# Performance work log

Measured on AMD Instinct MI355X. Metric: run time of the kernel, lower is better.

## Reference

```python
import jax, jax.numpy as jnp
import numpy as np

N_MODEL = 1024
N_HEADS = 16
KV_HEADS = 4
HEAD_DIM = N_MODEL // N_HEADS          # 64
KV_MODEL = HEAD_DIM * KV_HEADS         # 256
GROUPS = N_HEADS // KV_HEADS           # 4
B, S = 4, 2048


def _rmsnorm(x):
    return x * jax.lax.rsqrt(jnp.mean(x * x, axis=-1, keepdims=True) + 1e-6)


def _act_quant(x):
    # 8-bit absmax per-token quantization (BitNet b1.58)
    scale = 127.0 / jnp.clip(jnp.max(jnp.abs(x), axis=-1, keepdims=True), 1e-5)
    return jnp.clip(jnp.round(x * scale), -128.0, 127.0) / scale


def _weight_quant(w):
    # ternary absmean quantization
    scale = 1.0 / jnp.clip(jnp.mean(jnp.abs(w)), 1e-5)
    return jnp.clip(jnp.round(w * scale), -1.0, 1.0) / scale


def bitlinear(x, w, b):
    xn = _rmsnorm(x)
    xq = xn + jax.lax.stop_gradient(_act_quant(xn) - xn)   # STE
    wq = w + jax.lax.stop_gradient(_weight_quant(w) - w)   # STE
    return jnp.einsum('...i,oi->...o', xq, wq) + b


def setup_inputs() -> dict:
    key = jax.random.key(0)
    ks = jax.random.split(key, 11)
    sq = 1.0 / np.sqrt(N_MODEL)
    sk = 1.0 / np.sqrt(KV_MODEL)
    return {
        'query': jax.random.normal(ks[0], (B, S, N_MODEL), jnp.float32),
        'key':   jax.random.normal(ks[1], (B, S, N_MODEL), jnp.float32),
        'value': jax.random.normal(ks[2], (B, S, N_MODEL), jnp.float32),
        'Wq': jax.random.normal(ks[3], (N_MODEL, N_MODEL), jnp.float32) * sq,
        'bq': jnp.zeros((N_MODEL,), jnp.float32),
        'Wk': jax.random.normal(ks[4], (KV_MODEL, N_MODEL), jnp.float32) * sq,
        'bk': jnp.zeros((KV_MODEL,), jnp.float32),
        'Wv': jax.random.normal(ks[5], (KV_MODEL, N_MODEL), jnp.float32) * sq,
        'bv': jnp.zeros((KV_MODEL,), jnp.float32),
        'Wo': jax.random.normal(ks[6], (N_MODEL, KV_MODEL), jnp.float32) * sk,
        'bo': jnp.zeros((N_MODEL,), jnp.float32),
    }


def reference(query, key, value, Wq, bq, Wk, bk, Wv, bv, Wo, bo):
    b = query.shape[0]
    Q = bitlinear(query, Wq, bq)   # [b, n, n_model]
    K = bitlinear(key,   Wk, bk)   # [b, s, kv_model]
    V = bitlinear(value, Wv, bv)   # [b, s, kv_model]

    # [b, h, n, d] layouts
    Q = Q.reshape(b, -1, N_HEADS, HEAD_DIM).transpose(0, 2, 1, 3)
    K = K.reshape(b, -1, KV_HEADS, HEAD_DIM).transpose(0, 2, 1, 3)
    V = V.reshape(b, -1, KV_HEADS, HEAD_DIM).transpose(0, 2, 1, 3)

    # group query heads: [b, g, kv_h, n, d]
    Qg = Q.reshape(b, KV_HEADS, GROUPS, -1, HEAD_DIM).transpose(0, 2, 1, 3, 4)
    # NOTE: faithful to the module, the einsum output has no 'g' axis,
    # so the grouped query heads are SUMMED over g.
    energy = jnp.einsum('bghnd,bhsd->bhns', Qg, K)  # [b, kv_h, n, s]

    scale = jnp.sqrt(jnp.float32(HEAD_DIM))
    attention = jax.nn.softmax(energy / scale, axis=-1)
    x = jnp.einsum('bhns,bhsd->bhnd', attention, V)  # [b, kv_h, n, d]
    x = x.transpose(0, 2, 1, 3).reshape(b, -1, KV_MODEL)
    x = bitlinear(x, Wo, bo)       # [b, n, n_model]
    return (x, attention)
```

## Files before the change

### kernel.cpp

```cpp
#include <hip/hip_runtime.h>
#include <stdint.h>

#define N_MODELC 1024
#define KV_MODELC 256
#define BATCH 4
#define SEQ 2048
#define NTOK (BATCH*SEQ)

typedef __attribute__((ext_vector_type(4))) float f32x4;
typedef __attribute__((ext_vector_type(4))) int   i32x4;
typedef __attribute__((ext_vector_type(8))) short s16x8;

__device__ __forceinline__ unsigned short f2bf(float f){
  unsigned u = __builtin_bit_cast(unsigned, f);
  u = (u + 0x7FFFu + ((u>>16)&1u)) >> 16;
  return (unsigned short)u;
}

__global__ __launch_bounds__(256) void k_actquant1024(
    const float* __restrict__ xq_in, const float* __restrict__ xk_in, const float* __restrict__ xv_in,
    int8_t* __restrict__ q8q, int8_t* __restrict__ q8k, int8_t* __restrict__ q8v,
    float* __restrict__ scq, float* __restrict__ sck, float* __restrict__ scv)
{
  int row = blockIdx.x, which = blockIdx.y, t = threadIdx.x;
  const float* x = (which==0)?xq_in:(which==1)?xk_in:xv_in;
  int8_t* q8 = (which==0)?q8q:(which==1)?q8k:q8v;
  float* sc = (which==0)?scq:(which==1)?sck:scv;
  const float* xr = x + (size_t)row*N_MODELC;
  float4 v = reinterpret_cast<const float4*>(xr)[t];
  float ss = v.x*v.x + v.y*v.y + v.z*v.z + v.w*v.w;
  float am = fmaxf(fmaxf(fabsf(v.x),fabsf(v.y)), fmaxf(fabsf(v.z),fabsf(v.w)));
  #pragma unroll
  for (int m=32;m;m>>=1){ ss += __shfl_xor(ss,m,64); am = fmaxf(am, __shfl_xor(am,m,64)); }
  __shared__ float red[8];
  int wid = t>>6;
  if ((t&63)==0){ red[wid]=ss; red[4+wid]=am; }
  __syncthreads();
  ss = red[0]+red[1]+red[2]+red[3];
  am = fmaxf(fmaxf(red[4],red[5]), fmaxf(red[6],red[7]));
  float rinv = rsqrtf(ss*(1.0f/N_MODELC) + 1e-6f);
  float clipv = fmaxf(am*rinv, 1e-5f);
  float qs = 127.0f/clipv;
  float fsc = rinv*qs;
  char4 o;
  o.x = (signed char)(int)fminf(127.f, fmaxf(-128.f, rintf(v.x*fsc)));
  o.y = (signed char)(int)fminf(127.f, fmaxf(-128.f, rintf(v.y*fsc)));
  o.z = (signed char)(int)fminf(127.f, fmaxf(-128.f, rintf(v.z*fsc)));
  o.w = (signed char)(int)fminf(127.f, fmaxf(-128.f, rintf(v.w*fsc)));
  reinterpret_cast<char4*>(q8 + (size_t)row*N_MODELC)[t] = o;
  if (t==0) sc[row] = clipv*(1.0f/127.0f);
}

__global__ __launch_bounds__(64) void k_actquant256(
    const float* __restrict__ X, int8_t* __restrict__ q8, float* __restrict__ sc)
{
  int row = blockIdx.x, l = threadIdx.x;
  float4 v = reinterpret_cast<const float4*>(X + (size_t)row*KV_MODELC)[l];
  float ss = v.x*v.x + v.y*v.y + v.z*v.z + v.w*v.w;
  float am = fmaxf(fmaxf(fabsf(v.x),fabsf(v.y)), fmaxf(fabsf(v.z),fabsf(v.w)));
  #pragma unroll
  for (int m=32;m;m>>=1){ ss += __shfl_xor(ss,m,64); am = fmaxf(am, __shfl_xor(am,m,64)); }
  float rinv = rsqrtf(ss*(1.0f/KV_MODELC) + 1e-6f);
  float clipv = fmaxf(am*rinv, 1e-5f);
  float qs = 127.0f/clipv;
  float fsc = rinv*qs;
  char4 o;
  o.x = (signed char)(int)fminf(127.f, fmaxf(-128.f, rintf(v.x*fsc)));
  o.y = (signed char)(int)fminf(127.f, fmaxf(-128.f, rintf(v.y*fsc)));
  o.z = (signed char)(int)fminf(127.f, fmaxf(-128.f, rintf(v.z*fsc)));
  o.w = (signed char)(int)fminf(127.f, fmaxf(-128.f, rintf(v.w*fsc)));
  reinterpret_cast<char4*>(q8 + (size_t)row*KV_MODELC)[l] = o;
  if (l==0) sc[row] = clipv*(1.0f/127.0f);
}

__global__ __launch_bounds__(256) void k_wabs_partial(
    const float* __restrict__ Wq, const float* __restrict__ Wk,
    const float* __restrict__ Wv, const float* __restrict__ Wo, float* __restrict__ partial)
{
  int mat = blockIdx.y;
  const float* w = (mat==0)?Wq:(mat==1)?Wk:(mat==2)?Wv:Wo;
  int n = (mat==0)?(N_MODELC*N_MODELC):(KV_MODELC*N_MODELC);
  float s = 0.f;
  for (int i = blockIdx.x*256 + threadIdx.x; i < n; i += 256*256) s += fabsf(w[i]);
  #pragma unroll
  for (int m=32;m;m>>=1) s += __shfl_xor(s,m,64);
  __shared__ float red[4];
  int wid = threadIdx.x>>6;
  if ((threadIdx.x&63)==0) red[wid]=s;
  __syncthreads();
  if (threadIdx.x==0) partial[mat*256 + blockIdx.x] = red[0]+red[1]+red[2]+red[3];
}

__global__ __launch_bounds__(256) void k_wfinal(const float* __restrict__ partial, float* __restrict__ wfac)
{
  int mat = blockIdx.x, t = threadIdx.x;
  float s = partial[mat*256 + t];
  #pragma unroll
  for (int m=32;m;m>>=1) s += __shfl_xor(s,m,64);
  __shared__ float red[4];
  int wid = t>>6;
  if ((t&63)==0) red[wid]=s;
  __syncthreads();
  if (t==0){
    float tot = red[0]+red[1]+red[2]+red[3];
    float n = (mat==0)?(float)(N_MODELC*N_MODELC):(float)(KV_MODELC*N_MODELC);
    wfac[mat] = fmaxf(tot/n, 1e-5f);
  }
}

__global__ __launch_bounds__(256) void k_tern(
    const float* __restrict__ Wq, const float* __restrict__ Wk,
    const float* __restrict__ Wv, const float* __restrict__ Wo,
    const float* __restrict__ wfac,
    int8_t* __restrict__ Wqs, int8_t* __restrict__ Wkt,
    int8_t* __restrict__ Wvt, int8_t* __restrict__ Wot)
{
  int mat = blockIdx.y;
  int idx = blockIdx.x*256 + threadIdx.x;
  if (mat==0){
    float s = 1.0f/wfac[0];
    int op = idx>>10, i = idx&1023;
    int kv = op>>6, d = op&63;
    int acc = 0;
    #pragma unroll
    for (int g=0; g<4; g++){
      float w = Wq[(size_t)(kv*256 + g*64 + d)*N_MODELC + i];
      float r = fminf(1.f, fmaxf(-1.f, rintf(w*s)));
      acc += (int)r;
    }
    Wqs[idx] = (int8_t)acc;
  } else {
    const float* w = (mat==1)?Wk:(mat==2)?Wv:Wo;
    int8_t* o = (mat==1)?Wkt:(mat==2)?Wvt:Wot;
    float s = 1.0f/wfac[mat];
    float r = fminf(1.f, fmaxf(-1.f, rintf(w[idx]*s)));
    o[idx] = (int8_t)r;
  }
}

template<int KDIM, int MODE>
__global__ __launch_bounds__(256) void k_gemm_i8(
    const int8_t* __restrict__ A, const int8_t* __restrict__ B,
    const float* __restrict__ rowscale, const float* __restrict__ wfac, int wfi,
    const float* __restrict__ bias, void* __restrict__ outp)
{
  int mb = blockIdx.x*64, nb = blockIdx.y*64;
  int w = threadIdx.x>>6, l = threadIdx.x&63, lr = l&15, lk = l>>4;
  const int8_t* Ap = A + (size_t)(mb + w*16 + lr)*KDIM + lk*16;
  const int8_t* Bp = B + (size_t)(nb + lr)*KDIM + lk*16;
  i32x4 acc[4];
  #pragma unroll
  for (int f=0; f<4; f++) acc[f] = i32x4{0,0,0,0};
  #pragma unroll 4
  for (int kk=0; kk<KDIM; kk+=64){
    i32x4 a = *reinterpret_cast<const i32x4*>(Ap + kk);
    #pragma unroll
    for (int f=0; f<4; f++){
      i32x4 b = *reinterpret_cast<const i32x4*>(Bp + (size_t)f*16*KDIM + kk);
      acc[f] = __builtin_amdgcn_mfma_i32_16x16x64_i8(a, b, acc[f], 0, 0, 0);
    }
  }
  float wf = wfac[wfi];
  #pragma unroll
  for (int f=0; f<4; f++){
    int col = nb + f*16 + lr;
    float bval;
    if constexpr (MODE==0){
      int kv = col>>6, d = col&63;
      const float* bb = bias + kv*256 + d;
      bval = bb[0]+bb[64]+bb[128]+bb[192];
    } else {
      bval = bias[col];
    }
    #pragma unroll
    for (int r=0; r<4; r++){
      int row = mb + w*16 + lk*4 + r;
      float val = (float)acc[f][r] * (rowscale[row]*wf) + bval;
      if constexpr (MODE==0){
        ((unsigned short*)outp)[(size_t)row*KV_MODELC + col] = f2bf(0.125f*val);
      } else if constexpr (MODE==1){
        ((unsigned short*)outp)[(size_t)row*KV_MODELC + col] = f2bf(val);
      } else if constexpr (MODE==2){
        int bi = row>>11, s = row&2047;
        ((unsigned short*)outp)[((size_t)(bi*256 + col))*SEQ + s] = f2bf(val);
      } else {
        ((float*)outp)[(size_t)row*N_MODELC + col] = val;
      }
    }
  }
}

__global__ __launch_bounds__(256) void k_attn_pv(
    const unsigned short* __restrict__ Qs, const unsigned short* __restrict__ Kb,
    const unsigned short* __restrict__ VT,
    float* __restrict__ attn, float* __restrict__ X)
{
  __shared__ unsigned short plds[64][64];
  int bkv = blockIdx.y, b = bkv>>2, kv = bkv&3;
  int w = threadIdx.x>>6, l = threadIdx.x&63, lr = l&15, lk = l>>4;
  int brow = blockIdx.x*64;
  int rowt = brow + w*16;
  size_t tq = (size_t)(b*SEQ + rowt + lr)*KV_MODELC + kv*64 + lk*8;
  s16x8 qa0 = *reinterpret_cast<const s16x8*>(Qs + tq);
  s16x8 qa1 = *reinterpret_cast<const s16x8*>(Qs + tq + 32);
  const unsigned short* kbase = Kb + (size_t)b*SEQ*KV_MODELC + kv*64 + lk*8;
  const unsigned short* vbase = VT + ((size_t)(b*256 + kv*64))*SEQ;

  float m[4], ll[4];
  #pragma unroll
  for (int r=0;r<4;r++){ m[r] = -INFINITY; ll[r] = 0.f; }
  for (int st=0; st<SEQ; st+=16){
    const unsigned short* kp = kbase + (size_t)(st+lr)*KV_MODELC;
    s16x8 k0 = *reinterpret_cast<const s16x8*>(kp);
    s16x8 k1 = *reinterpret_cast<const s16x8*>(kp + 32);
    f32x4 acc = {0.f,0.f,0.f,0.f};
    acc = __builtin_amdgcn_mfma_f32_16x16x32_bf16(qa0, k0, acc, 0,0,0);
    acc = __builtin_amdgcn_mfma_f32_16x16x32_bf16(qa1, k1, acc, 0,0,0);
    #pragma unroll
    for (int r=0;r<4;r++){
      float e = acc[r];
      float mn = fmaxf(m[r], e);
      ll[r] = ll[r]*__expf(m[r]-mn) + __expf(e-mn);
      m[r] = mn;
    }
  }
  #pragma unroll
  for (int r=0;r<4;r++){
    #pragma unroll
    for (int mask=1; mask<16; mask<<=1){
      float om = __shfl_xor(m[r], mask, 64);
      float ol = __shfl_xor(ll[r], mask, 64);
      float mn = fmaxf(m[r], om);
      ll[r] = ll[r]*__expf(m[r]-mn) + ol*__expf(om-mn);
      m[r] = mn;
    }
  }
  float invl[4];
  #pragma unroll
  for (int r=0;r<4;r++) invl[r] = 1.0f/ll[r];

  float* arow = attn + (size_t)bkv*SEQ*SEQ + (size_t)brow*SEQ;
  f32x4 acco[4];
  #pragma unroll
  for (int dt=0; dt<4; dt++) acco[dt] = f32x4{0.f,0.f,0.f,0.f};
  int qw = w*16 + lk*4;
  int qr = w*16 + lr;
  int rsw = (qr&7)<<3;

  for (int st=0; st<SEQ; st+=64){
    #pragma unroll
    for (int sub=0; sub<4; sub++){
      int s0 = st + sub*16;
      const unsigned short* kp = kbase + (size_t)(s0+lr)*KV_MODELC;
      s16x8 k0 = *reinterpret_cast<const s16x8*>(kp);
      s16x8 k1 = *reinterpret_cast<const s16x8*>(kp + 32);
      f32x4 acc = {0.f,0.f,0.f,0.f};
      acc = __builtin_amdgcn_mfma_f32_16x16x32_bf16(qa0, k0, acc, 0,0,0);
      acc = __builtin_amdgcn_mfma_f32_16x16x32_bf16(qa1, k1, acc, 0,0,0);
      int slocal = sub*16 + lr;
      #pragma unroll
      for (int r=0;r<4;r++){
        float p = __expf(acc[r]-m[r])*invl[r];
        arow[(size_t)(qw + r)*SEQ + s0 + lr] = p;
        int sw = (slocal & 7) | ((((slocal>>3) ^ ((qw+r)&7)))<<3);
        plds[qw + r][sw] = f2bf(p);
      }
    }
    s16x8 a0 = *reinterpret_cast<const s16x8*>(&plds[qr][lk<<3 ^ rsw]);
    s16x8 a1 = *reinterpret_cast<const s16x8*>(&plds[qr][(4+lk)<<3 ^ rsw]);
    #pragma unroll
    for (int dt=0; dt<4; dt++){
      const unsigned short* vp = vbase + (size_t)(dt*16+lr)*SEQ + st + lk*8;
      s16x8 b0 = *reinterpret_cast<const s16x8*>(vp);
      s16x8 b1 = *reinterpret_cast<const s16x8*>(vp + 32);
      acco[dt] = __builtin_amdgcn_mfma_f32_16x16x32_bf16(a0, b0, acco[dt], 0,0,0);
      acco[dt] = __builtin_amdgcn_mfma_f32_16x16x32_bf16(a1, b1, acco[dt], 0,0,0);
    }
  }
  int token = b*SEQ + rowt + lk*4;
  #pragma unroll
  for (int dt=0; dt<4; dt++){
    #pragma unroll
    for (int r=0; r<4; r++){
      X[(size_t)(token + r)*KV_MODELC + kv*64 + dt*16 + lr] = acco[dt][r];
    }
  }
}

extern "C" void kernel_launch(void* const* d_in, const int* in_sizes, int n_in,
                              void* d_out, int out_size, void* d_ws, size_t ws_size,
                              hipStream_t stream)
{
  (void)in_sizes; (void)n_in; (void)out_size; (void)ws_size;
  const float* q  = (const float*)d_in[0];
  const float* k  = (const float*)d_in[1];
  const float* v  = (const float*)d_in[2];
  const float* Wq = (const float*)d_in[3];
  const float* bq = (const float*)d_in[4];
  const float* Wk = (const float*)d_in[5];
  const float* bk = (const float*)d_in[6];
  const float* Wv = (const float*)d_in[7];
  const float* bv = (const float*)d_in[8];
  const float* Wo = (const float*)d_in[9];
  const float* bo = (const float*)d_in[10];

  float* out_x = (float*)d_out;
  float* out_attn = out_x + (size_t)NTOK*N_MODELC;

  char* ws = (char*)d_ws;
  size_t off = 0;
  auto alloc = [&](size_t bytes)->void*{
    void* p = ws + off; off += (bytes + 255) & ~(size_t)255; return p;
  };
  int8_t* q8q = (int8_t*)alloc((size_t)NTOK*N_MODELC);
  int8_t* q8k = (int8_t*)alloc((size_t)NTOK*N_MODELC);
  int8_t* q8v = (int8_t*)alloc((size_t)NTOK*N_MODELC);
  int8_t* q8x = (int8_t*)alloc((size_t)NTOK*KV_MODELC);
  float* scq = (float*)alloc(NTOK*4);
  float* sck = (float*)alloc(NTOK*4);
  float* scv = (float*)alloc(NTOK*4);
  float* scx = (float*)alloc(NTOK*4);
  float* partial = (float*)alloc(4*256*4);
  float* wfac = (float*)alloc(256);
  int8_t* Wqs = (int8_t*)alloc(256*1024);
  int8_t* Wkt = (int8_t*)alloc(256*1024);
  int8_t* Wvt = (int8_t*)alloc(256*1024);
  int8_t* Wot = (int8_t*)alloc(1024*256);
  unsigned short* Qs = (unsigned short*)alloc((size_t)NTOK*KV_MODELC*2);
  unsigned short* Kb = (unsigned short*)alloc((size_t)NTOK*KV_MODELC*2);
  unsigned short* VT = (unsigned short*)alloc((size_t)NTOK*KV_MODELC*2);
  float* X = (float*)alloc((size_t)NTOK*KV_MODELC*4);

  hipLaunchKernelGGL(k_actquant1024, dim3(NTOK,3), dim3(256), 0, stream,
                     q,k,v, q8q,q8k,q8v, scq,sck,scv);
  hipLaunchKernelGGL(k_wabs_partial, dim3(256,4), dim3(256), 0, stream, Wq,Wk,Wv,Wo, partial);
  hipLaunchKernelGGL(k_wfinal, dim3(4), dim3(256), 0, stream, partial, wfac);
  hipLaunchKernelGGL(k_tern, dim3(1024,4), dim3(256), 0, stream,
                     Wq,Wk,Wv,Wo, wfac, Wqs,Wkt,Wvt,Wot);
  hipLaunchKernelGGL((k_gemm_i8<1024,0>), dim3(128,4), dim3(256), 0, stream,
                     q8q, Wqs, scq, wfac, 0, bq, (void*)Qs);
  hipLaunchKernelGGL((k_gemm_i8<1024,1>), dim3(128,4), dim3(256), 0, stream,
                     q8k, Wkt, sck, wfac, 1, bk, (void*)Kb);
  hipLaunchKernelGGL((k_gemm_i8<1024,2>), dim3(128,4), dim3(256), 0, stream,
                     q8v, Wvt, scv, wfac, 2, bv, (void*)VT);
  hipLaunchKernelGGL(k_attn_pv, dim3(32,16), dim3(256), 0, stream,
                     Qs, Kb, VT, out_attn, X);
  hipLaunchKernelGGL(k_actquant256, dim3(NTOK), dim3(64), 0, stream, X, q8x, scx);
  hipLaunchKernelGGL((k_gemm_i8<256,3>), dim3(128,16), dim3(256), 0, stream,
                     q8x, Wot, scx, wfac, 3, bo, (void*)out_x);
}
```

Before: 342.5 us.

## Split attention over key-sequence chunks into separate stats, PV and reduce kernels

The single attention kernel, launched on only 512 blocks, is split along the key sequence into 4 chunks. A first kernel computes per-chunk row max and sum-exp. A second kernel merges those stats, writes the attention probabilities and produces partial PV products for its chunk, and a third kernel sums the partials into X. This raises block count to 2048 to improve occupancy on a many-CU GPU, at the cost of extra launches, partial-buffer traffic and a reduction pass.

```diff
diff --git a/kernel.cpp b/kernel.cpp
--- a/kernel.cpp
+++ b/kernel.cpp
@@ -6,6 +6,8 @@
 #define BATCH 4
 #define SEQ 2048
 #define NTOK (BATCH*SEQ)
+#define NCHUNK 4
+#define CHUNK (SEQ/NCHUNK)
 
 typedef __attribute__((ext_vector_type(4))) float f32x4;
 typedef __attribute__((ext_vector_type(4))) int   i32x4;
@@ -190,13 +192,66 @@
   }
 }
 
-__global__ __launch_bounds__(256) void k_attn_pv(
+__global__ __launch_bounds__(256) void k_attn1(
+    const unsigned short* __restrict__ Qs, const unsigned short* __restrict__ Kb,
+    float* __restrict__ mpart, float* __restrict__ lpart)
+{
+  int bkv = blockIdx.y, b = bkv>>2, kv = bkv&3;
+  int c = blockIdx.z;
+  int w = threadIdx.x>>6, l = threadIdx.x&63, lr = l&15, lk = l>>4;
+  int rowt = blockIdx.x*64 + w*16;
+  size_t tq = (size_t)(b*SEQ + rowt + lr)*KV_MODELC + kv*64 + lk*8;
+  s16x8 qa0 = *reinterpret_cast<const s16x8*>(Qs + tq);
+  s16x8 qa1 = *reinterpret_cast<const s16x8*>(Qs + tq + 32);
+  const unsigned short* kbase = Kb + (size_t)b*SEQ*KV_MODELC + kv*64 + lk*8;
+  float m[4], ll[4];
+  #pragma unroll
+  for (int r=0;r<4;r++){ m[r] = -INFINITY; ll[r] = 0.f; }
+  for (int st=c*CHUNK; st<(c+1)*CHUNK; st+=16){
+    const unsigned short* kp = kbase + (size_t)(st+lr)*KV_MODELC;
+    s16x8 k0 = *reinterpret_cast<const s16x8*>(kp);
+    s16x8 k1 = *reinterpret_cast<const s16x8*>(kp + 32);
+    f32x4 acc = {0.f,0.f,0.f,0.f};
+    acc = __builtin_amdgcn_mfma_f32_16x16x32_bf16(qa0, k0, acc, 0,0,0);
+    acc = __builtin_amdgcn_mfma_f32_16x16x32_bf16(qa1, k1, acc, 0,0,0);
+    #pragma unroll
+    for (int r=0;r<4;r++){
+      float e = acc[r];
+      float mn = fmaxf(m[r], e);
+      ll[r] = ll[r]*__expf(m[r]-mn) + __expf(e-mn);
+      m[r] = mn;
+    }
+  }
+  #pragma unroll
+  for (int r=0;r<4;r++){
+    #pragma unroll
+    for (int mask=1; mask<16; mask<<=1){
+      float om = __shfl_xor(m[r], mask, 64);
+      float ol = __shfl_xor(ll[r], mask, 64);
+      float mn = fmaxf(m[r], om);
+      ll[r] = ll[r]*__expf(m[r]-mn) + ol*__expf(om-mn);
+      m[r] = mn;
+    }
+  }
+  if (lr==0){
+    #pragma unroll
+    for (int r=0;r<4;r++){
+      size_t idx = ((size_t)(c*16 + bkv))*SEQ + rowt + lk*4 + r;
+      mpart[idx] = m[r];
+      lpart[idx] = ll[r];
+    }
+  }
+}
+
+__global__ __launch_bounds__(256) void k_attn2(
     const unsigned short* __restrict__ Qs, const unsigned short* __restrict__ Kb,
     const unsigned short* __restrict__ VT,
-    float* __restrict__ attn, float* __restrict__ X)
+    const float* __restrict__ mpart, const float* __restrict__ lpart,
+    float* __restrict__ attn, float* __restrict__ pvpart)
 {
   __shared__ unsigned short plds[64][64];
   int bkv = blockIdx.y, b = bkv>>2, kv = bkv&3;
+  int c = blockIdx.z;
   int w = threadIdx.x>>6, l = threadIdx.x&63, lr = l&15, lk = l>>4;
   int brow = blockIdx.x*64;
   int rowt = brow + w*16;
@@ -206,38 +261,21 @@
   const unsigned short* kbase = Kb + (size_t)b*SEQ*KV_MODELC + kv*64 + lk*8;
   const unsigned short* vbase = VT + ((size_t)(b*256 + kv*64))*SEQ;
 
-  float m[4], ll[4];
-  #pragma unroll
-  for (int r=0;r<4;r++){ m[r] = -INFINITY; ll[r] = 0.f; }
-  for (int st=0; st<SEQ; st+=16){
-    const unsigned short* kp = kbase + (size_t)(st+lr)*KV_MODELC;
-    s16x8 k0 = *reinterpret_cast<const s16x8*>(kp);
-    s16x8 k1 = *reinterpret_cast<const s16x8*>(kp + 32);
-    f32x4 acc = {0.f,0.f,0.f,0.f};
-    acc = __builtin_amdgcn_mfma_f32_16x16x32_bf16(qa0, k0, acc, 0,0,0);
-    acc = __builtin_amdgcn_mfma_f32_16x16x32_bf16(qa1, k1, acc, 0,0,0);
-    #pragma unroll
-    for (int r=0;r<4;r++){
-      float e = acc[r];
-      float mn = fmaxf(m[r], e);
-      ll[r] = ll[r]*__expf(m[r]-mn) + __expf(e-mn);
-      m[r] = mn;
-    }
-  }
+  float m[4], invl[4];
   #pragma unroll
   for (int r=0;r<4;r++){
-    #pragma unroll
-    for (int mask=1; mask<16; mask<<=1){
-      float om = __shfl_xor(m[r], mask, 64);
-      float ol = __shfl_xor(ll[r], mask, 64);
-      float mn = fmaxf(m[r], om);
-      ll[r] = ll[r]*__expf(m[r]-mn) + ol*__expf(om-mn);
-      m[r] = mn;
-    }
-  }
-  float invl[4];
-  #pragma unroll
-  for (int r=0;r<4;r++) invl[r] = 1.0f/ll[r];
+    int row = rowt + lk*4 + r;
+    float M = -INFINITY, L = 0.f;
+    #pragma unroll
+    for (int cc=0; cc<NCHUNK; cc++){
+      size_t idx = ((size_t)(cc*16 + bkv))*SEQ + row;
+      float mm = mpart[idx], lw = lpart[idx];
+      float mn = fmaxf(M, mm);
+      L = L*__expf(M-mn) + lw*__expf(mm-mn);
+      M = mn;
+    }
+    m[r] = M; invl[r] = 1.0f/L;
+  }
 
   float* arow = attn + (size_t)bkv*SEQ*SEQ + (size_t)brow*SEQ;
   f32x4 acco[4];
@@ -247,7 +285,7 @@
   int qr = w*16 + lr;
   int rsw = (qr&7)<<3;
 
-  for (int st=0; st<SEQ; st+=64){
+  for (int st=c*CHUNK; st<(c+1)*CHUNK; st+=64){
     #pragma unroll
     for (int sub=0; sub<4; sub++){
       int s0 = st + sub*16;
@@ -266,8 +304,8 @@
         plds[qw + r][sw] = f2bf(p);
       }
     }
-    s16x8 a0 = *reinterpret_cast<const s16x8*>(&plds[qr][lk<<3 ^ rsw]);
-    s16x8 a1 = *reinterpret_cast<const s16x8*>(&plds[qr][(4+lk)<<3 ^ rsw]);
+    s16x8 a0 = *reinterpret_cast<const s16x8*>(&plds[qr][(lk<<3) ^ rsw]);
+    s16x8 a1 = *reinterpret_cast<const s16x8*>(&plds[qr][((4+lk)<<3) ^ rsw]);
     #pragma unroll
     for (int dt=0; dt<4; dt++){
       const unsigned short* vp = vbase + (size_t)(dt*16+lr)*SEQ + st + lk*8;
@@ -277,14 +315,29 @@
       acco[dt] = __builtin_amdgcn_mfma_f32_16x16x32_bf16(a1, b1, acco[dt], 0,0,0);
     }
   }
-  int token = b*SEQ + rowt + lk*4;
   #pragma unroll
   for (int dt=0; dt<4; dt++){
     #pragma unroll
     for (int r=0; r<4; r++){
-      X[(size_t)(token + r)*KV_MODELC + kv*64 + dt*16 + lr] = acco[dt][r];
-    }
-  }
+      int row = rowt + lk*4 + r;
+      pvpart[(((size_t)(c*16 + bkv))*SEQ + row)*64 + dt*16 + lr] = acco[dt][r];
+    }
+  }
+}
+
+__global__ __launch_bounds__(256) void k_pvsum(
+    const float* __restrict__ pvpart, float* __restrict__ X)
+{
+  size_t idx = (size_t)blockIdx.x*256 + threadIdx.x;
+  int d = idx & 63;
+  int row = (int)((idx>>6) & (SEQ-1));
+  int bkv = (int)(idx >> 17);
+  float s = 0.f;
+  #pragma unroll
+  for (int c=0; c<NCHUNK; c++)
+    s += pvpart[(((size_t)(c*16 + bkv))*SEQ + row)*64 + d];
+  int b = bkv>>2, kv = bkv&3;
+  X[((size_t)(b*SEQ + row))*KV_MODELC + kv*64 + d] = s;
 }
 
 extern "C" void kernel_launch(void* const* d_in, const int* in_sizes, int n_in,
@@ -330,6 +383,9 @@
   unsigned short* Kb = (unsigned short*)alloc((size_t)NTOK*KV_MODELC*2);
   unsigned short* VT = (unsigned short*)alloc((size_t)NTOK*KV_MODELC*2);
   float* X = (float*)alloc((size_t)NTOK*KV_MODELC*4);
+  float* mpart = (float*)alloc((size_t)NCHUNK*16*SEQ*4);
+  float* lpart = (float*)alloc((size_t)NCHUNK*16*SEQ*4);
+  float* pvpart = (float*)alloc((size_t)NCHUNK*16*SEQ*64*4);
 
   hipLaunchKernelGGL(k_actquant1024, dim3(NTOK,3), dim3(256), 0, stream,
                      q,k,v, q8q,q8k,q8v, scq,sck,scv);
@@ -343,8 +399,12 @@
                      q8k, Wkt, sck, wfac, 1, bk, (void*)Kb);
   hipLaunchKernelGGL((k_gemm_i8<1024,2>), dim3(128,4), dim3(256), 0, stream,
                      q8v, Wvt, scv, wfac, 2, bv, (void*)VT);
-  hipLaunchKernelGGL(k_attn_pv, dim3(32,16), dim3(256), 0, stream,
-                     Qs, Kb, VT, out_attn, X);
+  hipLaunchKernelGGL(k_attn1, dim3(32,16,NCHUNK), dim3(256), 0, stream,
+                     Qs, Kb, mpart, lpart);
+  hipLaunchKernelGGL(k_attn2, dim3(32,16,NCHUNK), dim3(256), 0, stream,
+                     Qs, Kb, VT, mpart, lpart, out_attn, pvpart);
+  hipLaunchKernelGGL(k_pvsum, dim3(16*SEQ*64/256), dim3(256), 0, stream,
+                     pvpart, X);
   hipLaunchKernelGGL(k_actquant256, dim3(NTOK), dim3(64), 0, stream, X, q8x, scx);
   hipLaunchKernelGGL((k_gemm_i8<256,3>), dim3(128,16), dim3(256), 0, stream,
                      q8x, Wot, scx, wfac, 3, bo, (void*)out_x);
```

Measured after the change: 351.1 us. 2.5% more time.
